# Performance work log

Hardware: AMD Instinct MI355X
Metric: run time of the kernel (lower is better)

Reference implementation:

```python
import jax, jax.numpy as jnp
import numpy as np

TAU = 10.0
K = 5
EPS = 1e-8


def get_patches(x, k):
    # x: [B, C, H, W] -> [B, C, k, k, L] with L=(H-k+1)*(W-k+1), stride-1 sliding window
    B, C, H, W = x.shape
    Hp, Wp = H - k + 1, W - k + 1
    p = jnp.stack(
        [jnp.stack([x[:, :, i:i + Hp, j:j + Wp] for j in range(k)], axis=2) for i in range(k)],
        axis=2,
    )  # [B, C, k, k, Hp, Wp]
    return p.reshape(B, C, k, k, Hp * Wp)


def setup_inputs() -> dict:
    key = jax.random.key(0)
    k1, k2 = jax.random.split(key)
    semantic_features = jax.random.normal(k1, (2, 32, 192, 192), dtype=jnp.float32)
    depth_gt = jax.random.uniform(k2, (2, 1, 192, 192), dtype=jnp.float32)
    return {"semantic_features": semantic_features, "depth_gt": depth_gt}


def reference(semantic_features, depth_gt):
    k = K
    c = k // 2
    sp = get_patches(semantic_features, k)            # [B, C, k, k, L]
    dp = get_patches(1.0 / (depth_gt + 1e-6), k)      # [B, 1, k, k, L]
    sem_center = sp[:, :, c, c, :]                    # [B, C, L]
    depth_center = dp[:, 0, c, c, :]                  # [B, L]

    depth_diff = jnp.abs(depth_center[:, None, None, :] - dp[:, 0])           # [B, k, k, L]
    sem_diff = jnp.sqrt(jnp.sum((sem_center[:, :, None, None, :] - sp) ** 2, axis=1))  # [B, k, k, L]

    depth_diff = jnp.maximum(depth_diff, EPS)
    sem_diff = jnp.maximum(sem_diff, EPS)

    loss0 = (jnp.expm1(-depth_diff / TAU) + 1.0) * (jnp.expm1(-sem_diff ** 2) + 1.0)  # [B, k, k, L]

    m = (depth_diff > EPS) & (sem_diff > EPS)         # [B, k, k, L]
    pos = dp[:, 0] > 0.0                              # [B, k, k, L]
    # faithful to torch broadcasting: [B,k,k,L] & [B,1,k,k,L] -> [B,B,k,k,L]
    mask = m[None] & pos[:, None]                     # [B, B, k, k, L]
    loss = loss0[None] * mask.astype(loss0.dtype)     # [B, B, k, k, L]

    center_mask = jnp.ones((k, k), loss.dtype).at[c, c].set(0.0)
    loss = loss * center_mask[None, None, :, :, None]
    return jnp.mean(jnp.mean(loss, axis=(2, 3)))
```

## Files before the change

kernel.cpp:

```cpp
#include <hip/hip_runtime.h>
#include <math.h>


#define HP    188
#define IMW   192
#define NCH   32
#define TW    64
#define HWC   68
#define NR    5
#define PLANE (IMW * IMW)
#define NBLK  (3 * HP * 2)
#define NSLOT (8 * NR * HWC)
#define SPT   11

__device__ __forceinline__ unsigned bf16_bits(float f) {
    unsigned u = __float_as_uint(f);
    return (u + 0x7fffu + ((u >> 16) & 1u)) >> 16;
}
__device__ __forceinline__ float bf16_rne(float f) {
    unsigned u = __float_as_uint(f);
    u += 0x7fffu + ((u >> 16) & 1u);
    u &= 0xffff0000u;
    return __uint_as_float(u);
}
__device__ __forceinline__ float lo_f(unsigned p) { return __uint_as_float(p << 16); }
__device__ __forceinline__ float hi_f(unsigned p) { return __uint_as_float(p & 0xffff0000u); }

__global__ __launch_bounds__(256) void dgp_tiled(
    const float* __restrict__ S,
    const float* __restrict__ D,
    double* __restrict__ partials)
{
    __shared__ __align__(8) uint2 smp[8][NR][HWC];
    __shared__ float  rd[NR][HWC];
    __shared__ double wsum[4];

    const int tid = threadIdx.x;
    const int tx  = tid & 63;
    const int tg  = tid >> 6;

    const int l   = blockIdx.x;
    const int xcd = l & 7;
    const int g   = xcd * 141 + (l >> 3);
    const int c   = g / HP;
    const int oy  = g - c * HP;
    const int b   = c / 3;
    const int ox0 = (c - 3 * b) * TW;

    float dv[2];
#pragma unroll
    for (int s = 0; s < 2; ++s) {
        const int t = tid + 256 * s;
        float d = 1.0f;
        if (t < NR * HWC) {
            const int i   = t / HWC;
            const int col = t - i * HWC;
            const int gc  = ox0 + col;
            if (gc < IMW) d = D[(b * IMW + (oy + i)) * IMW + gc];
        }
        dv[s] = d;
    }
    float4 sv[SPT];
#pragma unroll
    for (int s = 0; s < SPT; ++s) {
        const int t = tid + 256 * s;
        float4 v = make_float4(0.f, 0.f, 0.f, 0.f);
        if (t < NSLOT) {
            const int q   = t / (NR * HWC);
            const int rem = t - q * (NR * HWC);
            const int i   = rem / HWC;
            const int col = rem - i * HWC;
            const int gc  = ox0 + col;
            if (gc < IMW) {
                const int base = ((b * NCH + 4 * q) * IMW + (oy + i)) * IMW + gc;
                v.x = S[base];
                v.y = S[base + PLANE];
                v.z = S[base + 2 * PLANE];
                v.w = S[base + 3 * PLANE];
            }
        }
        sv[s] = v;
    }

#pragma unroll
    for (int s = 0; s < 2; ++s) {
        const int t = tid + 256 * s;
        if (t < NR * HWC) {
            const int i   = t / HWC;
            const int col = t - i * HWC;
            rd[i][col] = 1.0f / (bf16_rne(dv[s]) + 1e-6f);
        }
    }
#pragma unroll
    for (int s = 0; s < SPT; ++s) {
        const int t = tid + 256 * s;
        if (t < NSLOT) {
            const int q   = t / (NR * HWC);
            const int rem = t - q * (NR * HWC);
            const int i   = rem / HWC;
            const int col = rem - i * HWC;
            const float4 v = sv[s];
            uint2 pk;
            pk.x = bf16_bits(v.x) | (__float_as_uint(bf16_rne(v.y)) & 0xffff0000u);
            pk.y = bf16_bits(v.z) | (__float_as_uint(bf16_rne(v.w)) & 0xffff0000u);
            smp[q][i][col] = pk;
        }
    }
    __syncthreads();

    double acc = 0.0;
    const int ox = ox0 + tx;
    if (ox < HP) {
        float cs[NCH];
#pragma unroll
        for (int q = 0; q < 8; ++q) {
            const uint2 p = smp[q][2][tx + 2];
            cs[4 * q + 0] = lo_f(p.x);
            cs[4 * q + 1] = hi_f(p.x);
            cs[4 * q + 2] = lo_f(p.y);
            cs[4 * q + 3] = hi_f(p.y);
        }
        const float rc = rd[2][tx + 2];

        for (int k = 0; k < 6; ++k) {
            int t = tg * 6 + k;
            t += (t >= 12);
            const int i = t / 5;
            const int j = t - 5 * i;

            float f0 = 0.f, f1 = 0.f, f2 = 0.f, f3 = 0.f;
#pragma unroll
            for (int q = 0; q < 8; ++q) {
                const uint2 p = smp[q][i][tx + j];
                const float t0 = cs[4 * q + 0] - lo_f(p.x);
                const float t1 = cs[4 * q + 1] - hi_f(p.x);
                const float t2 = cs[4 * q + 2] - lo_f(p.y);
                const float t3 = cs[4 * q + 3] - hi_f(p.y);
                f0 = fmaf(t0, t0, f0);
                f1 = fmaf(t1, t1, f1);
                f2 = fmaf(t2, t2, f2);
                f3 = fmaf(t3, t3, f3);
            }
            const float sq_fast = (f0 + f1) + (f2 + f3);

            if (sq_fast <= 18.001f) {
                const float rn = rd[i][tx + j];
                const float dd = fabsf(rc - rn);

                float r[8];
                {
#pragma clang fp contract(off)
#pragma unroll
                    for (int blk = 0; blk < 4; ++blk) {
                        const uint2 pe = smp[2 * blk][i][tx + j];
                        const uint2 po = smp[2 * blk + 1][i][tx + j];
                        float p;
                        p = cs[8 * blk + 0] - lo_f(pe.x); p = p * p; r[0] = blk ? r[0] + p : p;
                        p = cs[8 * blk + 1] - hi_f(pe.x); p = p * p; r[1] = blk ? r[1] + p : p;
                        p = cs[8 * blk + 2] - lo_f(pe.y); p = p * p; r[2] = blk ? r[2] + p : p;
                        p = cs[8 * blk + 3] - hi_f(pe.y); p = p * p; r[3] = blk ? r[3] + p : p;
                        p = cs[8 * blk + 4] - lo_f(po.x); p = p * p; r[4] = blk ? r[4] + p : p;
                        p = cs[8 * blk + 5] - hi_f(po.x); p = p * p; r[5] = blk ? r[5] + p : p;
                        p = cs[8 * blk + 6] - lo_f(po.y); p = p * p; r[6] = blk ? r[6] + p : p;
                        p = cs[8 * blk + 7] - hi_f(po.y); p = p * p; r[7] = blk ? r[7] + p : p;
                    }
                }
                const float sq = ((r[0] + r[1]) + (r[2] + r[3]))
                               + ((r[4] + r[5]) + (r[6] + r[7]));

                const float sd  = sqrtf(sq);
                const float ddc = fmaxf(dd, 1e-8f);
                const float sdc = fmaxf(sd, 1e-8f);

                if (ddc > 1e-8f && sdc > 1e-8f) {
                    const float s2 = sdc * sdc;
                    if (s2 <= 18.0f) {
                        const float ls = (float)expm1(-(double)s2) + 1.0f;
                        const float ad = -(ddc / 10.0f);
                        const float ld = (float)expm1((double)ad) + 1.0f;
                        acc += 2.0 * (double)(ld * ls);
                    }
                }
            }
        }
    }

#pragma unroll
    for (int off = 32; off > 0; off >>= 1)
        acc += __shfl_down(acc, off);
    if ((tid & 63) == 0) wsum[tid >> 6] = acc;
    __syncthreads();
    if (tid == 0)
        partials[l] = wsum[0] + wsum[1] + wsum[2] + wsum[3];
}

__global__ __launch_bounds__(256) void dgp_fin(
    const double* __restrict__ partials, float* __restrict__ out)
{
    const int tid = threadIdx.x;
    double acc = 0.0;
    for (int k = tid; k < NBLK; k += 256)
        acc += partials[k];
#pragma unroll
    for (int off = 32; off > 0; off >>= 1)
        acc += __shfl_down(acc, off);
    __shared__ double ws[4];
    if ((tid & 63) == 0) ws[tid >> 6] = acc;
    __syncthreads();
    if (tid == 0)
        out[0] = (float)((ws[0] + ws[1] + ws[2] + ws[3]) / 3534400.0);
}

extern "C" void kernel_launch(void* const* d_in, const int* in_sizes, int n_in,
                              void* d_out, int out_size, void* d_ws, size_t ws_size,
                              hipStream_t stream)
{
    const float* S = (const float*)d_in[0];
    const float* D = (const float*)d_in[1];
    if (n_in >= 2 && in_sizes[0] < in_sizes[1]) {
        S = (const float*)d_in[1];
        D = (const float*)d_in[0];
    }
    double* partials = (double*)d_ws;

    dgp_tiled<<<NBLK, 256, 0, stream>>>(S, D, partials);
    dgp_fin<<<1, 256, 0, stream>>>(partials, (float*)d_out);
}
```

Before: 74.07 us.

## Process two output rows per block to reuse staged halo rows

Each block now stages 6 input rows instead of 5 and computes two consecutive output rows, halving the block count (with padding blocks that write zero partials). This cuts redundant global loads and bf16 packing of overlapping halo rows, from 5 staged rows per output row down to 3. In exchange each thread holds more live values and the loop body doubles, which may raise register pressure, and the grid shrinks to about 568 blocks, which reduces parallelism.

New measurement: 73.46 us. About the same (-0.8%).

```diff
diff --git a/kernel.cpp b/kernel.cpp
--- a/kernel.cpp
+++ b/kernel.cpp
@@ -7,11 +7,13 @@
 #define NCH   32
 #define TW    64
 #define HWC   68
-#define NR    5
+#define NR2   6
+#define NYT   94
 #define PLANE (IMW * IMW)
-#define NBLK  (3 * HP * 2)
-#define NSLOT (8 * NR * HWC)
-#define SPT   11
+#define NWRK  (3 * NYT * 2)
+#define NBLK  568
+#define NSLOT (8 * NR2 * HWC)
+#define SPT   13
 
 __device__ __forceinline__ unsigned bf16_bits(float f) {
     unsigned u = __float_as_uint(f);
@@ -31,8 +33,8 @@
     const float* __restrict__ D,
     double* __restrict__ partials)
 {
-    __shared__ __align__(8) uint2 smp[8][NR][HWC];
-    __shared__ float  rd[NR][HWC];
+    __shared__ __align__(8) uint2 smp[8][NR2][HWC];
+    __shared__ float  rd[NR2][HWC];
     __shared__ double wsum[4];
 
     const int tid = threadIdx.x;
@@ -41,9 +43,13 @@
 
     const int l   = blockIdx.x;
     const int xcd = l & 7;
-    const int g   = xcd * 141 + (l >> 3);
-    const int c   = g / HP;
-    const int oy  = g - c * HP;
+    const int g   = xcd * 71 + (l >> 3);
+    if (g >= NWRK) {
+        if (tid == 0) partials[l] = 0.0;
+        return;
+    }
+    const int c   = g / NYT;
+    const int oy0 = (g - c * NYT) * 2;
     const int b   = c / 3;
     const int ox0 = (c - 3 * b) * TW;
 
@@ -52,11 +58,11 @@
     for (int s = 0; s < 2; ++s) {
         const int t = tid + 256 * s;
         float d = 1.0f;
-        if (t < NR * HWC) {
+        if (t < NR2 * HWC) {
             const int i   = t / HWC;
             const int col = t - i * HWC;
             const int gc  = ox0 + col;
-            if (gc < IMW) d = D[(b * IMW + (oy + i)) * IMW + gc];
+            if (gc < IMW) d = D[(b * IMW + (oy0 + i)) * IMW + gc];
         }
         dv[s] = d;
     }
@@ -66,13 +72,13 @@
         const int t = tid + 256 * s;
         float4 v = make_float4(0.f, 0.f, 0.f, 0.f);
         if (t < NSLOT) {
-            const int q   = t / (NR * HWC);
-            const int rem = t - q * (NR * HWC);
+            const int q   = t / (NR2 * HWC);
+            const int rem = t - q * (NR2 * HWC);
             const int i   = rem / HWC;
             const int col = rem - i * HWC;
             const int gc  = ox0 + col;
             if (gc < IMW) {
-                const int base = ((b * NCH + 4 * q) * IMW + (oy + i)) * IMW + gc;
+                const int base = ((b * NCH + 4 * q) * IMW + (oy0 + i)) * IMW + gc;
                 v.x = S[base];
                 v.y = S[base + PLANE];
                 v.z = S[base + 2 * PLANE];
@@ -85,7 +91,7 @@
 #pragma unroll
     for (int s = 0; s < 2; ++s) {
         const int t = tid + 256 * s;
-        if (t < NR * HWC) {
+        if (t < NR2 * HWC) {
             const int i   = t / HWC;
             const int col = t - i * HWC;
             rd[i][col] = 1.0f / (bf16_rne(dv[s]) + 1e-6f);
@@ -95,8 +101,8 @@
     for (int s = 0; s < SPT; ++s) {
         const int t = tid + 256 * s;
         if (t < NSLOT) {
-            const int q   = t / (NR * HWC);
-            const int rem = t - q * (NR * HWC);
+            const int q   = t / (NR2 * HWC);
+            const int rem = t - q * (NR2 * HWC);
             const int i   = rem / HWC;
             const int col = rem - i * HWC;
             const float4 v = sv[s];
@@ -111,74 +117,77 @@
     double acc = 0.0;
     const int ox = ox0 + tx;
     if (ox < HP) {
-        float cs[NCH];
-#pragma unroll
-        for (int q = 0; q < 8; ++q) {
-            const uint2 p = smp[q][2][tx + 2];
-            cs[4 * q + 0] = lo_f(p.x);
-            cs[4 * q + 1] = hi_f(p.x);
-            cs[4 * q + 2] = lo_f(p.y);
-            cs[4 * q + 3] = hi_f(p.y);
-        }
-        const float rc = rd[2][tx + 2];
-
-        for (int k = 0; k < 6; ++k) {
-            int t = tg * 6 + k;
-            t += (t >= 12);
-            const int i = t / 5;
-            const int j = t - 5 * i;
-
-            float f0 = 0.f, f1 = 0.f, f2 = 0.f, f3 = 0.f;
+#pragma unroll
+        for (int py = 0; py < 2; ++py) {
+            float cs[NCH];
 #pragma unroll
             for (int q = 0; q < 8; ++q) {
-                const uint2 p = smp[q][i][tx + j];
-                const float t0 = cs[4 * q + 0] - lo_f(p.x);
-                const float t1 = cs[4 * q + 1] - hi_f(p.x);
-                const float t2 = cs[4 * q + 2] - lo_f(p.y);
-                const float t3 = cs[4 * q + 3] - hi_f(p.y);
-                f0 = fmaf(t0, t0, f0);
-                f1 = fmaf(t1, t1, f1);
-                f2 = fmaf(t2, t2, f2);
-                f3 = fmaf(t3, t3, f3);
+                const uint2 p = smp[q][py + 2][tx + 2];
+                cs[4 * q + 0] = lo_f(p.x);
+                cs[4 * q + 1] = hi_f(p.x);
+                cs[4 * q + 2] = lo_f(p.y);
+                cs[4 * q + 3] = hi_f(p.y);
             }
-            const float sq_fast = (f0 + f1) + (f2 + f3);
-
-            if (sq_fast <= 18.001f) {
-                const float rn = rd[i][tx + j];
-                const float dd = fabsf(rc - rn);
-
-                float r[8];
-                {
+            const float rc = rd[py + 2][tx + 2];
+
+            for (int k = 0; k < 6; ++k) {
+                int t = tg * 6 + k;
+                t += (t >= 12);
+                const int i = py + t / 5;
+                const int j = t - 5 * (t / 5);
+
+                float f0 = 0.f, f1 = 0.f, f2 = 0.f, f3 = 0.f;
+#pragma unroll
+                for (int q = 0; q < 8; ++q) {
+                    const uint2 p = smp[q][i][tx + j];
+                    const float t0 = cs[4 * q + 0] - lo_f(p.x);
+                    const float t1 = cs[4 * q + 1] - hi_f(p.x);
+                    const float t2 = cs[4 * q + 2] - lo_f(p.y);
+                    const float t3 = cs[4 * q + 3] - hi_f(p.y);
+                    f0 = fmaf(t0, t0, f0);
+                    f1 = fmaf(t1, t1, f1);
+                    f2 = fmaf(t2, t2, f2);
+                    f3 = fmaf(t3, t3, f3);
+                }
+                const float sq_fast = (f0 + f1) + (f2 + f3);
+
+                if (sq_fast <= 18.001f) {
+                    const float rn = rd[i][tx + j];
+                    const float dd = fabsf(rc - rn);
+
+                    float r[8];
+                    {
 #pragma clang fp contract(off)
 #pragma unroll
-                    for (int blk = 0; blk < 4; ++blk) {
-                        const uint2 pe = smp[2 * blk][i][tx + j];
-                        const uint2 po = smp[2 * blk + 1][i][tx + j];
-                        float p;
-                        p = cs[8 * blk + 0] - lo_f(pe.x); p = p * p; r[0] = blk ? r[0] + p : p;
-                        p = cs[8 * blk + 1] - hi_f(pe.x); p = p * p; r[1] = blk ? r[1] + p : p;
-                        p = cs[8 * blk + 2] - lo_f(pe.y); p = p * p; r[2] = blk ? r[2] + p : p;
-                        p = cs[8 * blk + 3] - hi_f(pe.y); p = p * p; r[3] = blk ? r[3] + p : p;
-                        p = cs[8 * blk + 4] - lo_f(po.x); p = p * p; r[4] = blk ? r[4] + p : p;
-                        p = cs[8 * blk + 5] - hi_f(po.x); p = p * p; r[5] = blk ? r[5] + p : p;
-                        p = cs[8 * blk + 6] - lo_f(po.y); p = p * p; r[6] = blk ? r[6] + p : p;
-                        p = cs[8 * blk + 7] - hi_f(po.y); p = p * p; r[7] = blk ? r[7] + p : p;
+                        for (int blk = 0; blk < 4; ++blk) {
+                            const uint2 pe = smp[2 * blk][i][tx + j];
+                            const uint2 po = smp[2 * blk + 1][i][tx + j];
+                            float p;
+                            p = cs[8 * blk + 0] - lo_f(pe.x); p = p * p; r[0] = blk ? r[0] + p : p;
+                            p = cs[8 * blk + 1] - hi_f(pe.x); p = p * p; r[1] = blk ? r[1] + p : p;
+                            p = cs[8 * blk + 2] - lo_f(pe.y); p = p * p; r[2] = blk ? r[2] + p : p;
+                            p = cs[8 * blk + 3] - hi_f(pe.y); p = p * p; r[3] = blk ? r[3] + p : p;
+                            p = cs[8 * blk + 4] - lo_f(po.x); p = p * p; r[4] = blk ? r[4] + p : p;
+                            p = cs[8 * blk + 5] - hi_f(po.x); p = p * p; r[5] = blk ? r[5] + p : p;
+                            p = cs[8 * blk + 6] - lo_f(po.y); p = p * p; r[6] = blk ? r[6] + p : p;
+                            p = cs[8 * blk + 7] - hi_f(po.y); p = p * p; r[7] = blk ? r[7] + p : p;
+                        }
                     }
-                }
-                const float sq = ((r[0] + r[1]) + (r[2] + r[3]))
-                               + ((r[4] + r[5]) + (r[6] + r[7]));
-
-                const float sd  = sqrtf(sq);
-                const float ddc = fmaxf(dd, 1e-8f);
-                const float sdc = fmaxf(sd, 1e-8f);
-
-                if (ddc > 1e-8f && sdc > 1e-8f) {
-                    const float s2 = sdc * sdc;
-                    if (s2 <= 18.0f) {
-                        const float ls = (float)expm1(-(double)s2) + 1.0f;
-                        const float ad = -(ddc / 10.0f);
-                        const float ld = (float)expm1((double)ad) + 1.0f;
-                        acc += 2.0 * (double)(ld * ls);
+                    const float sq = ((r[0] + r[1]) + (r[2] + r[3]))
+                                   + ((r[4] + r[5]) + (r[6] + r[7]));
+
+                    const float sd  = sqrtf(sq);
+                    const float ddc = fmaxf(dd, 1e-8f);
+                    const float sdc = fmaxf(sd, 1e-8f);
+
+                    if (ddc > 1e-8f && sdc > 1e-8f) {
+                        const float s2 = sdc * sdc;
+                        if (s2 <= 18.0f) {
+                            const float ls = (float)expm1(-(double)s2) + 1.0f;
+                            const float ad = -(ddc / 10.0f);
+                            const float ld = (float)expm1((double)ad) + 1.0f;
+                            acc += 2.0 * (double)(ld * ls);
+                        }
                     }
                 }
             }
```
